# Optimization experiments

Hardware: AMD Instinct MI355X
Metric: run time of the kernel (lower is better)

## Reference

```python
import jax, jax.numpy as jnp
import numpy as np

B, CIN, COUT, H, W = 4, 256, 128, 64, 64

def conv1x1(x, w, b):
    # x: [B,C,H,W], w: [O,C], b: [O]
    return jnp.einsum('bchw,oc->bohw', x, w) + b[None, :, None, None]

def setup_inputs() -> dict:
    key = jax.random.key(0)
    ks = jax.random.split(key, 9)
    s_in = 1.0 / np.sqrt(CIN)
    s_out = 1.0 / np.sqrt(COUT)
    return {
        'x': jax.random.normal(ks[0], (B, CIN, H, W), dtype=jnp.float32),
        'w_theta': jax.random.normal(ks[1], (COUT, CIN), dtype=jnp.float32) * s_in,
        'b_theta': jax.random.normal(ks[2], (COUT,), dtype=jnp.float32) * s_in,
        'w_phi': jax.random.normal(ks[3], (COUT, CIN), dtype=jnp.float32) * s_in,
        'b_phi': jax.random.normal(ks[4], (COUT,), dtype=jnp.float32) * s_in,
        'w_g': jax.random.normal(ks[5], (COUT, CIN), dtype=jnp.float32) * s_in,
        'b_g': jax.random.normal(ks[6], (COUT,), dtype=jnp.float32) * s_in,
        'w_W': jax.random.normal(ks[7], (CIN, COUT), dtype=jnp.float32) * s_out,
        'b_W': jax.random.normal(ks[8], (CIN,), dtype=jnp.float32) * s_out,
    }

def reference(x, w_theta, b_theta, w_phi, b_phi, w_g, b_g, w_W, b_W):
    b, c, h, w = x.shape
    n = h * w
    co = w_theta.shape[0]
    theta_x = conv1x1(x, w_theta, b_theta).reshape(b, co, n).transpose(0, 2, 1)  # [B,N,Co]
    phi_x = conv1x1(x, w_phi, b_phi).reshape(b, co, n)                            # [B,Co,N]
    g_x = conv1x1(x, w_g, b_g).reshape(b, co, n).transpose(0, 2, 1)               # [B,N,Co]
    scores = jnp.einsum('bnc,bcm->bnm', theta_x, phi_x)                           # [B,N,N]
    attn = jax.nn.softmax(scores, axis=-1)
    y = jnp.einsum('bnm,bmc->bnc', attn, g_x)                                     # [B,N,Co]
    y = y.transpose(0, 2, 1).reshape(b, co, h, w)
    z = conv1x1(y, w_W, b_W) + x
    return z
```

## Files before the change

kernel.cpp:

```cpp
#include <hip/hip_runtime.h>

#define B_    4
#define C_    256
#define O_    128
#define N_    4096
#define THW   256
#define TILES 64

typedef __attribute__((ext_vector_type(8))) _Float16 f16x8;
typedef __attribute__((ext_vector_type(4))) float    f32x4;

struct __align__(8) us4 { unsigned short x, y, z, w; };

__device__ __forceinline__ float bf2f(unsigned short u) {
    unsigned v = ((unsigned)u) << 16;
    union { unsigned u; float f; } c; c.u = v; return c.f;
}
__device__ __forceinline__ unsigned short f2bf(float f) {
    union { float f; unsigned u; } c; c.f = f;
    unsigned r = c.u + 0x7fffu + ((c.u >> 16) & 1u);
    return (unsigned short)(r >> 16);
}
__device__ __forceinline__ unsigned short f2h(float f) {
    _Float16 h = (_Float16)f;
    union { _Float16 h; unsigned short s; } c; c.h = h; return c.s;
}
__device__ __forceinline__ float h2f(unsigned short s) {
    union { unsigned short s; _Float16 h; } c; c.s = s; return (float)c.h;
}

__device__ __forceinline__ void load4f(const void* base, size_t idx, int isf32, float o[4]) {
    if (isf32) {
        float4 v = *(const float4*)((const float*)base + idx);
        o[0] = v.x; o[1] = v.y; o[2] = v.z; o[3] = v.w;
    } else {
        us4 v = *(const us4*)((const unsigned short*)base + idx);
        o[0] = bf2f(v.x); o[1] = bf2f(v.y); o[2] = bf2f(v.z); o[3] = bf2f(v.w);
    }
}
__device__ __forceinline__ float load1f(const void* base, size_t idx, int isf32) {
    return isf32 ? ((const float*)base)[idx] : bf2f(((const unsigned short*)base)[idx]);
}

__global__ __launch_bounds__(256) void detect_kernel(
    const unsigned short* __restrict__ xu, int* __restrict__ flag)
{
    __shared__ int cnt;
    if (threadIdx.x == 0) cnt = 0;
    __syncthreads();
    int local = 0;
    for (int i = threadIdx.x; i < 4096; i += 256) {
        unsigned short u = xu[2 * i];
        int e = (u >> 7) & 0xFF;
        if (e == 0xFF || e >= 0x90 || (e > 0 && e <= 0x60)) local++;
    }
    atomicAdd(&cnt, local);
    __syncthreads();
    if (threadIdx.x == 0) *flag = (cnt > 1024) ? 1 : 0;
}

__global__ __launch_bounds__(256) void qkv_kernel(
    const void* __restrict__ x,
    const void* __restrict__ wt, const void* __restrict__ wp,
    const void* __restrict__ wg,
    const void* __restrict__ bt, const void* __restrict__ bp,
    const void* __restrict__ bg,
    const int*  __restrict__ flag,
    unsigned short* __restrict__ thph,
    unsigned short* __restrict__ gT)
{
    const int isf32 = *flag;
    const int jsel = blockIdx.y;
    const void* w  = jsel == 0 ? wt : (jsel == 1 ? wp : wg);
    const void* bi = jsel == 0 ? bt : (jsel == 1 ? bp : bg);
    const int b  = blockIdx.z;
    const int n0 = blockIdx.x * 64;
    const int tid  = threadIdx.x;
    const int wv   = tid >> 6, lane = tid & 63;
    const int quad = lane >> 4, l16 = lane & 15;

    __shared__ alignas(16) unsigned short smem[64 * 72 + 128 * 72];
    unsigned short (*As)[72] = (unsigned short(*)[72])smem;
    unsigned short (*Bs)[72] = (unsigned short(*)[72])(smem + 64 * 72);

    f32x4 acc[8];
    for (int i = 0; i < 8; i++) acc[i] = (f32x4)0.f;

    for (int kc = 0; kc < C_; kc += 64) {
        __syncthreads();
        for (int it = 0; it < 4; it++) {
            int l = it * 256 + tid;
            int c = l >> 4;
            int ng = l & 15;
            float v[4];
            load4f(x, (size_t)(b * C_ + kc + c) * N_ + n0 + ng * 4, isf32, v);
            int g = c >> 3, cl = c & 7;
            int swz = ((g ^ (ng & 7)) << 3) + cl;
            As[ng * 4 + 0][swz] = f2h(v[0]);
            As[ng * 4 + 1][swz] = f2h(v[1]);
            As[ng * 4 + 2][swz] = f2h(v[2]);
            As[ng * 4 + 3][swz] = f2h(v[3]);
        }
        for (int it = 0; it < 8; it++) {
            int l = it * 256 + tid;
            int j = l >> 4;
            int cg = l & 15;
            float v[4];
            load4f(w, (size_t)j * C_ + kc + cg * 4, isf32, v);
            Bs[j][cg * 4 + 0] = f2h(v[0]);
            Bs[j][cg * 4 + 1] = f2h(v[1]);
            Bs[j][cg * 4 + 2] = f2h(v[2]);
            Bs[j][cg * 4 + 3] = f2h(v[3]);
        }
        __syncthreads();
        for (int s = 0; s < 2; s++) {
            int row = wv * 16 + l16;
            int g2 = ((s * 4 + quad) ^ ((row >> 2) & 7)) << 3;
            f16x8 a = *(const f16x8*)&As[row][g2];
            for (int jt = 0; jt < 8; jt++) {
                f16x8 bb = *(const f16x8*)&Bs[jt * 16 + l16][s * 32 + quad * 8];
                acc[jt] = __builtin_amdgcn_mfma_f32_16x16x32_f16(a, bb, acc[jt], 0, 0, 0);
            }
        }
    }

    if (jsel < 2) {
        for (int jt = 0; jt < 8; jt++) {
            int j = jt * 16 + l16;
            float bias = load1f(bi, j, isf32);
            for (int r = 0; r < 4; r++) {
                int n = n0 + wv * 16 + quad * 4 + r;
                thph[(size_t)(b * N_ + n) * THW + jsel * O_ + j] = f2h(acc[jt][r] + bias);
            }
        }
    } else {
        unsigned short (*T)[68] = (unsigned short(*)[68])smem;
        __syncthreads();
        for (int jt = 0; jt < 8; jt++) {
            int j = jt * 16 + l16;
            float bias = load1f(bi, j, isf32);
            for (int r = 0; r < 4; r++) {
                int nl = wv * 16 + quad * 4 + r;
                T[j][nl] = f2h(acc[jt][r] + bias);
            }
        }
        __syncthreads();
        for (int it = 0; it < 8; it++) {
            int l = it * 256 + tid;
            int j = l >> 4;
            int ng = l & 15;
            *(us4*)(gT + ((size_t)(b * O_ + j)) * N_ + n0 + ng * 4) = *(const us4*)&T[j][ng * 4];
        }
    }
}

__global__ __launch_bounds__(512, 4) void attn_partial(
    const unsigned short* __restrict__ thph,
    const unsigned short* __restrict__ gT,
    unsigned short* __restrict__ partO,
    float* __restrict__ pm,
    float* __restrict__ pl,
    int S)
{
    const int b    = blockIdx.z;
    const int s_id = blockIdx.y;
    const int n0   = blockIdx.x * 128;
    const int tid  = threadIdx.x;
    const int wv   = tid >> 6, lane = tid & 63;
    const int quad = lane >> 4, l16 = lane & 15;

    const int t0 = (TILES * s_id) / S;
    const int t1 = (TILES * (s_id + 1)) / S;

    __shared__ alignas(16) unsigned short Ks[64][136];
    __shared__ alignas(16) unsigned short Gs[128][72];
    __shared__ alignas(16) unsigned short Ps[8][16][72];

    f16x8 qf[4];
    {
        int qrow = n0 + wv * 16 + l16;
        const unsigned short* qp = thph + (size_t)(b * N_ + qrow) * THW;
        for (int s = 0; s < 4; s++)
            qf[s] = *(const f16x8*)(qp + s * 32 + quad * 8);
    }

    f32x4 oacc[8];
    for (int i = 0; i < 8; i++) oacc[i] = (f32x4)0.f;
    float mstate = -INFINITY, lstate = 0.f;

    us4 kreg[4], greg[4];
    auto prefetch = [&](int mt) {
        int m0 = mt * 64;
        #pragma unroll
        for (int it = 0; it < 4; it++) {
            int l = it * 512 + tid;
            int mm = l >> 5, og = l & 31;
            kreg[it] = *(const us4*)(thph + (size_t)(b * N_ + m0 + mm) * THW + O_ + og * 4);
        }
        #pragma unroll
        for (int it = 0; it < 4; it++) {
            int l = it * 512 + tid;
            int o = l >> 4, ng = l & 15;
            greg[it] = *(const us4*)(gT + ((size_t)(b * O_ + o)) * N_ + m0 + ng * 4);
        }
    };
    prefetch(t0);

    for (int mt = t0; mt < t1; mt++) {
        __syncthreads();
        #pragma unroll
        for (int it = 0; it < 4; it++) {
            int l = it * 512 + tid;
            int mm = l >> 5, og = l & 31;
            *(us4*)&Ks[mm][og * 4] = kreg[it];
        }
        #pragma unroll
        for (int it = 0; it < 4; it++) {
            int l = it * 512 + tid;
            int o = l >> 4, ng = l & 15;
            *(us4*)&Gs[o][ng * 4] = greg[it];
        }
        __syncthreads();
        if (mt + 1 < t1) prefetch(mt + 1);

        f32x4 sacc[4];
        for (int kt = 0; kt < 4; kt++) sacc[kt] = (f32x4)0.f;
        for (int s = 0; s < 4; s++) {
            for (int kt = 0; kt < 4; kt++) {
                f16x8 kb = *(const f16x8*)&Ks[kt * 16 + l16][s * 32 + quad * 8];
                sacc[kt] = __builtin_amdgcn_mfma_f32_16x16x32_f16(kb, qf[s], sacc[kt], 0, 0, 0);
            }
        }

        float rm = fmaxf(fmaxf(fmaxf(sacc[0][0], sacc[0][1]), fmaxf(sacc[0][2], sacc[0][3])),
                         fmaxf(fmaxf(sacc[1][0], sacc[1][1]), fmaxf(sacc[1][2], sacc[1][3])));
        rm = fmaxf(rm, fmaxf(fmaxf(fmaxf(sacc[2][0], sacc[2][1]), fmaxf(sacc[2][2], sacc[2][3])),
                             fmaxf(fmaxf(sacc[3][0], sacc[3][1]), fmaxf(sacc[3][2], sacc[3][3]))));
        rm = fmaxf(rm, __shfl_xor(rm, 16));
        rm = fmaxf(rm, __shfl_xor(rm, 32));

        float mnew  = fmaxf(mstate, rm);
        float alpha = __expf(mstate - mnew);
        mstate = mnew;

        float rs = 0.f;
        #pragma unroll
        for (int kt = 0; kt < 4; kt++) {
            float p0 = __expf(sacc[kt][0] - mnew);
            float p1 = __expf(sacc[kt][1] - mnew);
            float p2 = __expf(sacc[kt][2] - mnew);
            float p3 = __expf(sacc[kt][3] - mnew);
            rs += (p0 + p1) + (p2 + p3);
            us4 pk;
            pk.x = f2h(p0); pk.y = f2h(p1); pk.z = f2h(p2); pk.w = f2h(p3);
            *(us4*)&Ps[wv][l16][kt * 16 + quad * 4] = pk;
        }
        rs += __shfl_xor(rs, 16);
        rs += __shfl_xor(rs, 32);
        lstate = lstate * alpha + rs;

        float av[4];
        #pragma unroll
        for (int r = 0; r < 4; r++) av[r] = __shfl(alpha, quad * 4 + r);
        #pragma unroll
        for (int jt = 0; jt < 8; jt++)
            #pragma unroll
            for (int r = 0; r < 4; r++) oacc[jt][r] *= av[r];

        for (int s = 0; s < 2; s++) {
            f16x8 pa = *(const f16x8*)&Ps[wv][l16][s * 32 + quad * 8];
            for (int jt = 0; jt < 8; jt++) {
                f16x8 gb = *(const f16x8*)&Gs[jt * 16 + l16][s * 32 + quad * 8];
                oacc[jt] = __builtin_amdgcn_mfma_f32_16x16x32_f16(pa, gb, oacc[jt], 0, 0, 0);
            }
        }
    }

    for (int r = 0; r < 4; r++) {
        int n = n0 + wv * 16 + quad * 4 + r;
        size_t rowb = ((size_t)(s_id * B_ + b) * N_ + n) * O_;
        for (int jt = 0; jt < 8; jt++)
            partO[rowb + jt * 16 + l16] = f2h(oacc[jt][r]);
    }
    if (quad == 0) {
        int n = n0 + wv * 16 + l16;
        pm[(size_t)(s_id * B_ + b) * N_ + n] = mstate;
        pl[(size_t)(s_id * B_ + b) * N_ + n] = lstate;
    }
}

__global__ __launch_bounds__(256) void merge_kernel(
    const unsigned short* __restrict__ partO,
    const float* __restrict__ pm, const float* __restrict__ pl,
    unsigned short* __restrict__ y,
    int S)
{
    int idx = blockIdx.x * 256 + threadIdx.x;
    int bn  = idx >> 5;
    int og  = idx & 31;
    const int BN = B_ * N_;

    float M = -INFINITY;
    for (int s = 0; s < S; s++) M = fmaxf(M, pm[(size_t)s * BN + bn]);
    float w[4];
    float L = 0.f;
    for (int s = 0; s < S; s++) {
        w[s] = __expf(pm[(size_t)s * BN + bn] - M);
        L += w[s] * pl[(size_t)s * BN + bn];
    }
    float inv = 1.0f / L;

    float a0 = 0.f, a1 = 0.f, a2 = 0.f, a3 = 0.f;
    for (int s = 0; s < S; s++) {
        us4 v = *(const us4*)(partO + ((size_t)s * BN + bn) * O_ + og * 4);
        a0 += h2f(v.x) * w[s];
        a1 += h2f(v.y) * w[s];
        a2 += h2f(v.z) * w[s];
        a3 += h2f(v.w) * w[s];
    }
    us4 r;
    r.x = f2h(a0 * inv); r.y = f2h(a1 * inv);
    r.z = f2h(a2 * inv); r.w = f2h(a3 * inv);
    *(us4*)(y + (size_t)bn * O_ + og * 4) = r;
}

__global__ __launch_bounds__(256) void out_kernel(
    const unsigned short* __restrict__ y,
    const void* __restrict__ wW,
    const void* __restrict__ bW,
    const void* __restrict__ x,
    const int*  __restrict__ flag,
    void* __restrict__ z)
{
    const int isf32 = *flag;
    const int b  = blockIdx.z;
    const int c0 = blockIdx.y * 64;
    const int n0 = blockIdx.x * 128;
    const int tid  = threadIdx.x;
    const int wv   = tid >> 6, lane = tid & 63;
    const int quad = lane >> 4, l16 = lane & 15;

    __shared__ alignas(16) unsigned short Ys[128][136];
    __shared__ alignas(16) unsigned short Ws[64][136];

    for (int it = 0; it < 16; it++) {
        int l = it * 256 + tid;
        int nn = l >> 5;
        int og = l & 31;
        us4 v = *(const us4*)(y + (size_t)(b * N_ + n0 + nn) * O_ + og * 4);
        *(us4*)&Ys[nn][og * 4] = v;
    }
    for (int it = 0; it < 8; it++) {
        int l = it * 256 + tid;
        int cc = l >> 5;
        int og = l & 31;
        float v[4];
        load4f(wW, (size_t)(c0 + cc) * O_ + og * 4, isf32, v);
        Ws[cc][og * 4 + 0] = f2h(v[0]);
        Ws[cc][og * 4 + 1] = f2h(v[1]);
        Ws[cc][og * 4 + 2] = f2h(v[2]);
        Ws[cc][og * 4 + 3] = f2h(v[3]);
    }
    __syncthreads();

    f32x4 acc[8];
    for (int i = 0; i < 8; i++) acc[i] = (f32x4)0.f;
    for (int s = 0; s < 4; s++) {
        f16x8 a = *(const f16x8*)&Ws[wv * 16 + l16][s * 32 + quad * 8];
        for (int nt = 0; nt < 8; nt++) {
            f16x8 bb = *(const f16x8*)&Ys[nt * 16 + l16][s * 32 + quad * 8];
            acc[nt] = __builtin_amdgcn_mfma_f32_16x16x32_f16(a, bb, acc[nt], 0, 0, 0);
        }
    }
    for (int r = 0; r < 4; r++) {
        int c = c0 + wv * 16 + quad * 4 + r;
        float bias = load1f(bW, c, isf32);
        for (int nt = 0; nt < 8; nt++) {
            int n = n0 + nt * 16 + l16;
            size_t idx = (size_t)(b * C_ + c) * N_ + n;
            float zv = acc[nt][r] + bias + load1f(x, idx, isf32);
            if (isf32) ((float*)z)[idx] = zv;
            else       ((unsigned short*)z)[idx] = f2bf(zv);
        }
    }
}

extern "C" void kernel_launch(void* const* d_in, const int* in_sizes, int n_in,
                              void* d_out, int out_size, void* d_ws, size_t ws_size,
                              hipStream_t stream) {
    const void* x  = d_in[0];
    const void* wt = d_in[1];
    const void* bt = d_in[2];
    const void* wp = d_in[3];
    const void* bp = d_in[4];
    const void* wg = d_in[5];
    const void* bg = d_in[6];
    const void* wW = d_in[7];
    const void* bW = d_in[8];

    const size_t base = 64 + 8388608  + 4194304 ;
    const size_t per_split = 4194304  + 131072 ;
    int S = 4;
    while (S > 1 && base + (size_t)S * per_split > ws_size) S--;

    char* p = (char*)d_ws;
    int* flag = (int*)p;                    p += 64;
    unsigned short* thph = (unsigned short*)p;  p += 8388608;
    unsigned short* gT   = (unsigned short*)p;  p += 4194304;
    unsigned short* partO = (unsigned short*)p; p += (size_t)S * 4194304;
    float* pm = (float*)p;                  p += (size_t)S * 65536;
    float* pl = (float*)p;
    unsigned short* y = gT;

    detect_kernel<<<1, 256, 0, stream>>>((const unsigned short*)x, flag);

    dim3 g1(N_ / 64, 3, B_);
    qkv_kernel<<<g1, 256, 0, stream>>>(x, wt, wp, wg, bt, bp, bg, flag, thph, gT);

    dim3 g2(N_ / 128, S, B_);
    attn_partial<<<g2, 512, 0, stream>>>(thph, gT, partO, pm, pl, S);

    merge_kernel<<<(B_ * N_ * 32) / 256, 256, 0, stream>>>(partO, pm, pl, y, S);

    dim3 g3(N_ / 128, C_ / 64, B_);
    out_kernel<<<g3, 256, 0, stream>>>(y, wW, bW, x, flag, d_out);
}
```

Baseline: 186.7 us.

## Give each attention wave two query groups to reuse K/G LDS fragments

The attention kernel now runs 4 waves of 256 threads, each handling 32 query rows as two 16-row groups instead of one. Each K and G fragment read from LDS then feeds two MFMAs, halving LDS read traffic per MFMA. The PV product swaps operands so the output lands transposed, which gives per-row alpha scaling without shuffles and 8-byte vectorised partial-output stores. Global-to-LDS staging uses 16-byte loads, at the cost of more VGPRs per thread (double accumulators and Q fragments) and fewer threads per block.

Result: faster. 182.2 us (-2.4%).

```diff
diff --git a/kernel.cpp b/kernel.cpp
--- a/kernel.cpp
+++ b/kernel.cpp
@@ -154,7 +154,7 @@
     }
 }
 
-__global__ __launch_bounds__(512, 4) void attn_partial(
+__global__ __launch_bounds__(256, 2) void attn_partial(
     const unsigned short* __restrict__ thph,
     const unsigned short* __restrict__ gT,
     unsigned short* __restrict__ partO,
@@ -174,118 +174,135 @@
 
     __shared__ alignas(16) unsigned short Ks[64][136];
     __shared__ alignas(16) unsigned short Gs[128][72];
-    __shared__ alignas(16) unsigned short Ps[8][16][72];
-
-    f16x8 qf[4];
-    {
-        int qrow = n0 + wv * 16 + l16;
-        const unsigned short* qp = thph + (size_t)(b * N_ + qrow) * THW;
+    __shared__ alignas(16) unsigned short Ps[4][32][72];
+
+    const int wq0 = n0 + wv * 32;
+
+    f16x8 qf[2][4];
+    #pragma unroll
+    for (int qg = 0; qg < 2; qg++) {
+        const unsigned short* qp = thph + (size_t)(b * N_ + wq0 + qg * 16 + l16) * THW;
+        #pragma unroll
         for (int s = 0; s < 4; s++)
-            qf[s] = *(const f16x8*)(qp + s * 32 + quad * 8);
-    }
-
-    f32x4 oacc[8];
-    for (int i = 0; i < 8; i++) oacc[i] = (f32x4)0.f;
-    float mstate = -INFINITY, lstate = 0.f;
-
-    us4 kreg[4], greg[4];
+            qf[qg][s] = *(const f16x8*)(qp + s * 32 + quad * 8);
+    }
+
+    f32x4 oacc[2][8];
+    #pragma unroll
+    for (int qg = 0; qg < 2; qg++)
+        #pragma unroll
+        for (int i = 0; i < 8; i++) oacc[qg][i] = (f32x4)0.f;
+    float mst[2] = { -INFINITY, -INFINITY };
+    float lst[2] = { 0.f, 0.f };
+
+    const int krow = tid >> 4, kog = tid & 15;
+    const int grow = tid >> 3, gng = tid & 7;
+    const unsigned short* kb_g = thph + (size_t)(b * N_ + krow) * THW + O_ + kog * 8;
+    const unsigned short* gb_g = gT + ((size_t)(b * O_ + grow)) * N_ + gng * 8;
+
+    f16x8 kreg[4], greg[4];
     auto prefetch = [&](int mt) {
         int m0 = mt * 64;
         #pragma unroll
-        for (int it = 0; it < 4; it++) {
-            int l = it * 512 + tid;
-            int mm = l >> 5, og = l & 31;
-            kreg[it] = *(const us4*)(thph + (size_t)(b * N_ + m0 + mm) * THW + O_ + og * 4);
-        }
-        #pragma unroll
-        for (int it = 0; it < 4; it++) {
-            int l = it * 512 + tid;
-            int o = l >> 4, ng = l & 15;
-            greg[it] = *(const us4*)(gT + ((size_t)(b * O_ + o)) * N_ + m0 + ng * 4);
-        }
+        for (int it = 0; it < 4; it++)
+            kreg[it] = *(const f16x8*)(kb_g + (size_t)(m0 + it * 16) * THW);
+        #pragma unroll
+        for (int it = 0; it < 4; it++)
+            greg[it] = *(const f16x8*)(gb_g + m0 + (size_t)it * 32 * N_);
     };
     prefetch(t0);
 
     for (int mt = t0; mt < t1; mt++) {
         __syncthreads();
         #pragma unroll
-        for (int it = 0; it < 4; it++) {
-            int l = it * 512 + tid;
-            int mm = l >> 5, og = l & 31;
-            *(us4*)&Ks[mm][og * 4] = kreg[it];
-        }
-        #pragma unroll
-        for (int it = 0; it < 4; it++) {
-            int l = it * 512 + tid;
-            int o = l >> 4, ng = l & 15;
-            *(us4*)&Gs[o][ng * 4] = greg[it];
-        }
+        for (int it = 0; it < 4; it++)
+            *(f16x8*)&Ks[krow + it * 16][kog * 8] = kreg[it];
+        #pragma unroll
+        for (int it = 0; it < 4; it++)
+            *(f16x8*)&Gs[grow + it * 32][gng * 8] = greg[it];
         __syncthreads();
         if (mt + 1 < t1) prefetch(mt + 1);
 
-        f32x4 sacc[4];
-        for (int kt = 0; kt < 4; kt++) sacc[kt] = (f32x4)0.f;
+        f32x4 sacc[2][4];
+        #pragma unroll
+        for (int qg = 0; qg < 2; qg++)
+            #pragma unroll
+            for (int kt = 0; kt < 4; kt++) sacc[qg][kt] = (f32x4)0.f;
+        #pragma unroll
         for (int s = 0; s < 4; s++) {
+            #pragma unroll
             for (int kt = 0; kt < 4; kt++) {
                 f16x8 kb = *(const f16x8*)&Ks[kt * 16 + l16][s * 32 + quad * 8];
-                sacc[kt] = __builtin_amdgcn_mfma_f32_16x16x32_f16(kb, qf[s], sacc[kt], 0, 0, 0);
-            }
-        }
-
-        float rm = fmaxf(fmaxf(fmaxf(sacc[0][0], sacc[0][1]), fmaxf(sacc[0][2], sacc[0][3])),
-                         fmaxf(fmaxf(sacc[1][0], sacc[1][1]), fmaxf(sacc[1][2], sacc[1][3])));
-        rm = fmaxf(rm, fmaxf(fmaxf(fmaxf(sacc[2][0], sacc[2][1]), fmaxf(sacc[2][2], sacc[2][3])),
-                             fmaxf(fmaxf(sacc[3][0], sacc[3][1]), fmaxf(sacc[3][2], sacc[3][3]))));
-        rm = fmaxf(rm, __shfl_xor(rm, 16));
-        rm = fmaxf(rm, __shfl_xor(rm, 32));
-
-        float mnew  = fmaxf(mstate, rm);
-        float alpha = __expf(mstate - mnew);
-        mstate = mnew;
-
-        float rs = 0.f;
-        #pragma unroll
-        for (int kt = 0; kt < 4; kt++) {
-            float p0 = __expf(sacc[kt][0] - mnew);
-            float p1 = __expf(sacc[kt][1] - mnew);
-            float p2 = __expf(sacc[kt][2] - mnew);
-            float p3 = __expf(sacc[kt][3] - mnew);
-            rs += (p0 + p1) + (p2 + p3);
-            us4 pk;
-            pk.x = f2h(p0); pk.y = f2h(p1); pk.z = f2h(p2); pk.w = f2h(p3);
-            *(us4*)&Ps[wv][l16][kt * 16 + quad * 4] = pk;
-        }
-        rs += __shfl_xor(rs, 16);
-        rs += __shfl_xor(rs, 32);
-        lstate = lstate * alpha + rs;
-
-        float av[4];
-        #pragma unroll
-        for (int r = 0; r < 4; r++) av[r] = __shfl(alpha, quad * 4 + r);
-        #pragma unroll
-        for (int jt = 0; jt < 8; jt++)
+                sacc[0][kt] = __builtin_amdgcn_mfma_f32_16x16x32_f16(kb, qf[0][s], sacc[0][kt], 0, 0, 0);
+                sacc[1][kt] = __builtin_amdgcn_mfma_f32_16x16x32_f16(kb, qf[1][s], sacc[1][kt], 0, 0, 0);
+            }
+        }
+
+        #pragma unroll
+        for (int qg = 0; qg < 2; qg++) {
+            float rm = fmaxf(
+                fmaxf(fmaxf(fmaxf(sacc[qg][0][0], sacc[qg][0][1]), fmaxf(sacc[qg][0][2], sacc[qg][0][3])),
+                      fmaxf(fmaxf(sacc[qg][1][0], sacc[qg][1][1]), fmaxf(sacc[qg][1][2], sacc[qg][1][3]))),
+                fmaxf(fmaxf(fmaxf(sacc[qg][2][0], sacc[qg][2][1]), fmaxf(sacc[qg][2][2], sacc[qg][2][3])),
+                      fmaxf(fmaxf(sacc[qg][3][0], sacc[qg][3][1]), fmaxf(sacc[qg][3][2], sacc[qg][3][3]))));
+            rm = fmaxf(rm, __shfl_xor(rm, 16));
+            rm = fmaxf(rm, __shfl_xor(rm, 32));
+
+            float mnew  = fmaxf(mst[qg], rm);
+            float alpha = __expf(mst[qg] - mnew);
+            mst[qg] = mnew;
+
+            float rs = 0.f;
+            unsigned short* prow = &Ps[wv][qg * 16 + l16][quad * 4];
             #pragma unroll
-            for (int r = 0; r < 4; r++) oacc[jt][r] *= av[r];
-
+            for (int kt = 0; kt < 4; kt++) {
+                float p0 = __expf(sacc[qg][kt][0] - mnew);
+                float p1 = __expf(sacc[qg][kt][1] - mnew);
+                float p2 = __expf(sacc[qg][kt][2] - mnew);
+                float p3 = __expf(sacc[qg][kt][3] - mnew);
+                rs += (p0 + p1) + (p2 + p3);
+                us4 pk;
+                pk.x = f2h(p0); pk.y = f2h(p1); pk.z = f2h(p2); pk.w = f2h(p3);
+                *(us4*)(prow + kt * 16) = pk;
+            }
+            rs += __shfl_xor(rs, 16);
+            rs += __shfl_xor(rs, 32);
+            lst[qg] = lst[qg] * alpha + rs;
+
+            #pragma unroll
+            for (int jt = 0; jt < 8; jt++) oacc[qg][jt] *= alpha;
+        }
+
+        #pragma unroll
         for (int s = 0; s < 2; s++) {
-            f16x8 pa = *(const f16x8*)&Ps[wv][l16][s * 32 + quad * 8];
+            f16x8 pb0 = *(const f16x8*)&Ps[wv][l16][s * 32 + quad * 8];
+            f16x8 pb1 = *(const f16x8*)&Ps[wv][16 + l16][s * 32 + quad * 8];
+            #pragma unroll
             for (int jt = 0; jt < 8; jt++) {
-                f16x8 gb = *(const f16x8*)&Gs[jt * 16 + l16][s * 32 + quad * 8];
-                oacc[jt] = __builtin_amdgcn_mfma_f32_16x16x32_f16(pa, gb, oacc[jt], 0, 0, 0);
-            }
-        }
-    }
-
-    for (int r = 0; r < 4; r++) {
-        int n = n0 + wv * 16 + quad * 4 + r;
+                f16x8 ga = *(const f16x8*)&Gs[jt * 16 + l16][s * 32 + quad * 8];
+                oacc[0][jt] = __builtin_amdgcn_mfma_f32_16x16x32_f16(ga, pb0, oacc[0][jt], 0, 0, 0);
+                oacc[1][jt] = __builtin_amdgcn_mfma_f32_16x16x32_f16(ga, pb1, oacc[1][jt], 0, 0, 0);
+            }
+        }
+    }
+
+    #pragma unroll
+    for (int qg = 0; qg < 2; qg++) {
+        int n = wq0 + qg * 16 + l16;
         size_t rowb = ((size_t)(s_id * B_ + b) * N_ + n) * O_;
-        for (int jt = 0; jt < 8; jt++)
-            partO[rowb + jt * 16 + l16] = f2h(oacc[jt][r]);
-    }
-    if (quad == 0) {
-        int n = n0 + wv * 16 + l16;
-        pm[(size_t)(s_id * B_ + b) * N_ + n] = mstate;
-        pl[(size_t)(s_id * B_ + b) * N_ + n] = lstate;
+        #pragma unroll
+        for (int jt = 0; jt < 8; jt++) {
+            us4 v;
+            v.x = f2h(oacc[qg][jt][0]);
+            v.y = f2h(oacc[qg][jt][1]);
+            v.z = f2h(oacc[qg][jt][2]);
+            v.w = f2h(oacc[qg][jt][3]);
+            *(us4*)(partO + rowb + jt * 16 + quad * 4) = v;
+        }
+        if (quad == 0) {
+            pm[(size_t)(s_id * B_ + b) * N_ + n] = mst[qg];
+            pl[(size_t)(s_id * B_ + b) * N_ + n] = lst[qg];
+        }
     }
 }
 
@@ -418,7 +435,7 @@
     qkv_kernel<<<g1, 256, 0, stream>>>(x, wt, wp, wg, bt, bp, bg, flag, thph, gT);
 
     dim3 g2(N_ / 128, S, B_);
-    attn_partial<<<g2, 512, 0, stream>>>(thph, gT, partO, pm, pl, S);
+    attn_partial<<<g2, 256, 0, stream>>>(thph, gT, partO, pm, pl, S);
 
     merge_kernel<<<(B_ * N_ * 32) / 256, 256, 0, stream>>>(partO, pm, pl, y, S);
 
```
